# Kernel optimization log

Hardware: AMD Instinct MI355X
Metric: run time of the kernel (lower is better)

The kernel has to match this reference:

```python
import jax, jax.numpy as jnp
import numpy as np

CONTEXT_LENGTH = 4096
INPUT_LENGTH = 1024
N_EMBED = 512
HEAD_SIZE = 64
BATCH = 8


def _prefix_causal_mask(T):
    # A=ones(IL,IL), B=zeros(IL,non), C=ones(non,IL), D=tril(non,non)
    il = INPUT_LENGTH
    non = CONTEXT_LENGTH - il
    top = jnp.concatenate([jnp.ones((il, il)), jnp.zeros((il, non))], axis=1)
    bot = jnp.concatenate([jnp.ones((non, il)), jnp.tril(jnp.ones((non, non)))], axis=1)
    E = jnp.concatenate([top, bot], axis=0)
    return E[:T, :T]


def setup_inputs() -> dict:
    key = jax.random.key(0)
    kx, kq, kk, kv = jax.random.split(key, 4)
    scale = N_EMBED ** -0.5
    return {
        "x": jax.random.normal(kx, (BATCH, CONTEXT_LENGTH, N_EMBED), dtype=jnp.float32),
        "Wq": jax.random.normal(kq, (N_EMBED, HEAD_SIZE), dtype=jnp.float32) * scale,
        "Wk": jax.random.normal(kk, (N_EMBED, HEAD_SIZE), dtype=jnp.float32) * scale,
        "Wv": jax.random.normal(kv, (N_EMBED, HEAD_SIZE), dtype=jnp.float32) * scale,
    }


def reference(x, Wq, Wk, Wv):
    B, T, C = x.shape
    q = x @ Wq  # [B,T,h]
    k = x @ Wk  # [B,T,h]
    v = x @ Wv  # [B,T,h]
    # NOTE: original scales by C**-0.5 with C = n_embed (not head_size)
    wei = jnp.einsum("bth,bsh->bts", q, k) * (C ** -0.5)  # [B,T,T]
    mask = _prefix_causal_mask(T)  # [T,T], 1 = visible
    wei = jnp.where(mask == 0, jnp.float32(-jnp.inf), wei)
    wei = jax.nn.softmax(wei, axis=-1)
    # dropout p=0.0 (eval): identity
    return jnp.einsum("bts,bsh->bth", wei, v)  # [B,T,h]
```

## Files before the change

### kernel.cpp

```cpp
#include <hip/hip_runtime.h>
#include <hip/hip_bf16.h>


typedef short short8 __attribute__((ext_vector_type(8)));
typedef float floatx4 __attribute__((ext_vector_type(4)));

static __device__ __forceinline__ unsigned short f2b(float f) {
  unsigned u = __float_as_uint(f);
  unsigned r = (u + 0x7fffu + ((u >> 16) & 1u)) >> 16;
  return (unsigned short)r;
}

static __device__ __forceinline__ unsigned pkbf(float lo, float hi) {
  __hip_bfloat162 t = __float22bfloat162_rn(make_float2(lo, hi));
  unsigned d;
  __builtin_memcpy(&d, &t, 4);
  return d;
}

union S8U {
  short8 s;
  unsigned u[4];
};

__global__ __launch_bounds__(256) void wtrans(
    const float* __restrict__ Wq, const float* __restrict__ Wk,
    const float* __restrict__ Wv, unsigned short* __restrict__ Wtf) {
  int o = blockIdx.x * 256 + threadIdx.x;
  int e = o & 7;
  int ln = (o >> 3) & 63;
  int jg = o >> 9;
  int ks = jg / 12;
  int j = jg % 12;
  int m = j >> 2;
  int n = (j & 3) * 16 + (ln & 15);
  int k = ks * 32 + (ln >> 4) * 8 + e;
  const float* W = (m == 0) ? Wq : (m == 1) ? Wk : Wv;
  Wtf[o] = f2b(W[k * 64 + n]);
}

__global__ __launch_bounds__(256, 3) void proj(
    const float* __restrict__ x, const unsigned short* __restrict__ Wtf,
    unsigned short* __restrict__ q, unsigned short* __restrict__ Kf,
    unsigned short* __restrict__ Vf) {
  __shared__ float Cc[2][12][16][17];

  const int tid = threadIdx.x;
  const int lane = tid & 63;
  const int w = tid >> 6;
  const int u = lane & 15;
  const int qd = lane >> 4;
  const int pr = w >> 1;
  const int p = w & 1;
  const int g0 = blockIdx.x * 32;

  floatx4 acc[12];
#pragma unroll
  for (int j = 0; j < 12; ++j) acc[j] = (floatx4)0.0f;

  const float* xr = x + (size_t)(g0 + pr * 16 + u) * 512;

  for (int it = 0; it < 8; ++it) {
    const int ks = p + it * 2;
    floatx4 x0 = *reinterpret_cast<const floatx4*>(&xr[ks * 32 + qd * 8]);
    floatx4 x1 = *reinterpret_cast<const floatx4*>(&xr[ks * 32 + qd * 8 + 4]);
    S8U a;
    a.u[0] = pkbf(x0[0], x0[1]);
    a.u[1] = pkbf(x0[2], x0[3]);
    a.u[2] = pkbf(x1[0], x1[1]);
    a.u[3] = pkbf(x1[2], x1[3]);
#pragma unroll
    for (int j = 0; j < 12; ++j) {
      short8 bfr = *reinterpret_cast<const short8*>(&Wtf[(size_t)(ks * 12 + j) * 512 + lane * 8]);
      acc[j] = __builtin_amdgcn_mfma_f32_16x16x32_bf16(a.s, bfr, acc[j], 0, 0, 0);
    }
  }

  if (p == 1) {
#pragma unroll
    for (int j = 0; j < 12; ++j)
#pragma unroll
      for (int r = 0; r < 4; ++r)
        Cc[pr][j][qd * 4 + r][u] = acc[j][r];
  }
  __syncthreads();
  if (p == 0) {
#pragma unroll
    for (int j = 0; j < 12; ++j)
#pragma unroll
      for (int r = 0; r < 4; ++r)
        acc[j][r] += Cc[pr][j][qd * 4 + r][u];

    const float cexp = 0.04419417382415922f * 1.4426950408889634f;
    const int rbase = g0 + pr * 16;
    const int b = rbase >> 12;
    const int t = rbase & 4095;
    const int kt = t >> 6;
    const int sb = ((blockIdx.x & 1) << 1) + pr;
    const int sp = blockIdx.x & 1;
    unsigned short* kfb = Kf + ((size_t)(b * 64 + kt)) * 4096;
    unsigned short* vfb = Vf + ((size_t)(b * 64 + kt)) * 4096;

#pragma unroll
    for (int j = 0; j < 4; ++j)
#pragma unroll
      for (int r = 0; r < 4; ++r) {
        q[(size_t)(rbase + qd * 4 + r) * 64 + j * 16 + u] = f2b(acc[j][r] * cexp);
        {
          int kh = j >> 1;
          int qd_f = ((j & 1) << 1) + (u >> 3);
          kfb[(size_t)(kh * 4 + sb) * 512 + (qd_f * 16 + (qd * 4 + r)) * 8 + (u & 7)] =
              f2b(acc[4 + j][r]);
        }
        {
          int qd_f = pr * 2 + (qd >> 1);
          int e = ((qd & 1) << 2) + r;
          vfb[(size_t)(sp * 4 + j) * 512 + (qd_f * 16 + u) * 8 + e] = f2b(acc[8 + j][r]);
        }
      }
  }
}

__global__ __launch_bounds__(256, 2) void attn(
    const unsigned short* __restrict__ q, const unsigned short* __restrict__ Kf,
    const unsigned short* __restrict__ Vf, float* __restrict__ Op,
    float* __restrict__ Lp) {
  __shared__ unsigned Pb[4][4][64][4];
  __shared__ float OcA[64][68];
  __shared__ float OcB[64][68];
  __shared__ float Lc[4][64];

  const int tid = threadIdx.x;
  const int lane = tid & 63;
  const int w = tid >> 6;
  const int u = lane & 15;
  const int qd = lane >> 4;

  const int bx = blockIdx.x;
  const int b = bx & 7;
  const int s = bx >> 3;

  const int ts = (s * 2200) >> 6;
  const int te = ((s + 1) * 2200) >> 6;

  const unsigned short* qp = q + (size_t)b * 4096 * 64;
  const unsigned short* kfp = Kf + (size_t)b * 64 * 4096;
  const unsigned short* vfp = Vf + (size_t)b * 64 * 4096;

  int qt = 0, cq = 0;
  while (cq + ((qt < 16) ? 16 : (qt + 1)) <= ts) {
    cq += (qt < 16) ? 16 : (qt + 1);
    ++qt;
  }

  int tcur = ts;
  while (tcur < te) {
    const int tq = (qt < 16) ? 16 : (qt + 1);
    const int a = tcur - cq;
    const int bnd = (tq < te - cq) ? tq : (te - cq);
    int k0 = (cq * 64) / 2200;
    while ((((k0 + 1) * 2200) >> 6) <= cq) ++k0;
    const int o = s - k0;
    const int g0 = qt * 64;
    const int diagkt = (qt >= 16) ? qt : -1;

    short8 qB[4][2];
#pragma unroll
    for (int nb = 0; nb < 4; ++nb)
#pragma unroll
      for (int kh = 0; kh < 2; ++kh)
        qB[nb][kh] = *reinterpret_cast<const short8*>(
            &qp[(size_t)(g0 + nb * 16 + u) * 64 + kh * 32 + qd * 8]);

    floatx4 OT[4][4];
#pragma unroll
    for (int mb = 0; mb < 4; ++mb)
#pragma unroll
      for (int nb = 0; nb < 4; ++nb) OT[mb][nb] = (floatx4)0.0f;
    float L[4] = {0.f, 0.f, 0.f, 0.f};

    for (int kt = a + w; kt < bnd; kt += 4) {
      const unsigned short* kb = kfp + (size_t)kt * 4096;
      const unsigned short* vb = vfp + (size_t)kt * 4096;
      short8 kA[8];
#pragma unroll
      for (int f = 0; f < 8; ++f)
        kA[f] = *reinterpret_cast<const short8*>(&kb[(size_t)f * 512 + lane * 8]);
      const bool diag = (kt == diagkt);

#pragma unroll
      for (int sp = 0; sp < 2; ++sp) {
        short8 vA[4];
#pragma unroll
        for (int mb = 0; mb < 4; ++mb)
          vA[mb] = *reinterpret_cast<const short8*>(
              &vb[(size_t)(sp * 4 + mb) * 512 + lane * 8]);

        floatx4 ST[2][4];
#pragma unroll
        for (int sbb = 0; sbb < 2; ++sbb)
#pragma unroll
          for (int nb = 0; nb < 4; ++nb) ST[sbb][nb] = (floatx4)0.0f;
#pragma unroll
        for (int kh = 0; kh < 2; ++kh)
#pragma unroll
          for (int sbb = 0; sbb < 2; ++sbb)
#pragma unroll
            for (int nb = 0; nb < 4; ++nb)
              ST[sbb][nb] = __builtin_amdgcn_mfma_f32_16x16x32_bf16(
                  kA[kh * 4 + sp * 2 + sbb], qB[nb][kh], ST[sbb][nb], 0, 0, 0);

        if (diag) {
#pragma unroll
          for (int sbb = 0; sbb < 2; ++sbb)
#pragma unroll
            for (int nb = 0; nb < 4; ++nb)
#pragma unroll
              for (int r = 0; r < 4; ++r) {
                int sl = (sp * 2 + sbb) * 16 + qd * 4 + r;
                int qr = nb * 16 + u;
                if (sl > qr) ST[sbb][nb][r] = -__builtin_inff();
              }
        }

#pragma unroll
        for (int sbb = 0; sbb < 2; ++sbb)
#pragma unroll
          for (int nb = 0; nb < 4; ++nb) {
#pragma unroll
            for (int r = 0; r < 4; ++r)
              ST[sbb][nb][r] = __builtin_amdgcn_exp2f(ST[sbb][nb][r]);
            L[nb] += (ST[sbb][nb][0] + ST[sbb][nb][1]) + (ST[sbb][nb][2] + ST[sbb][nb][3]);
            unsigned lo = pkbf(ST[sbb][nb][0], ST[sbb][nb][1]);
            unsigned hi = pkbf(ST[sbb][nb][2], ST[sbb][nb][3]);
            int dl = (sbb * 2 + (qd >> 1)) * 16 + u;
            int d0 = (qd & 1) * 2;
            *reinterpret_cast<uint2*>(&Pb[w][nb][dl][d0]) = make_uint2(lo, hi);
          }

#pragma unroll
        for (int nb = 0; nb < 4; ++nb) {
          short8 pB = *reinterpret_cast<const short8*>(&Pb[w][nb][lane][0]);
#pragma unroll
          for (int mb = 0; mb < 4; ++mb)
            OT[mb][nb] = __builtin_amdgcn_mfma_f32_16x16x32_bf16(vA[mb], pB, OT[mb][nb], 0, 0, 0);
        }
      }
    }

#pragma unroll
    for (int nb = 0; nb < 4; ++nb) {
      L[nb] += __shfl_xor(L[nb], 16);
      L[nb] += __shfl_xor(L[nb], 32);
    }
    if (lane < 16) {
#pragma unroll
      for (int nb = 0; nb < 4; ++nb) Lc[w][nb * 16 + lane] = L[nb];
    }

    if (w == 1) {
#pragma unroll
      for (int mb = 0; mb < 4; ++mb)
#pragma unroll
        for (int nb = 0; nb < 4; ++nb)
          *reinterpret_cast<floatx4*>(&OcA[nb * 16 + u][mb * 16 + qd * 4]) = OT[mb][nb];
    }
    if (w == 3) {
#pragma unroll
      for (int mb = 0; mb < 4; ++mb)
#pragma unroll
        for (int nb = 0; nb < 4; ++nb)
          *reinterpret_cast<floatx4*>(&OcB[nb * 16 + u][mb * 16 + qd * 4]) = OT[mb][nb];
    }
    __syncthreads();
    if (w == 0) {
#pragma unroll
      for (int mb = 0; mb < 4; ++mb)
#pragma unroll
        for (int nb = 0; nb < 4; ++nb)
          OT[mb][nb] += *reinterpret_cast<const floatx4*>(&OcA[nb * 16 + u][mb * 16 + qd * 4]);
    }
    if (w == 2) {
#pragma unroll
      for (int mb = 0; mb < 4; ++mb)
#pragma unroll
        for (int nb = 0; nb < 4; ++nb) {
          OT[mb][nb] += *reinterpret_cast<const floatx4*>(&OcB[nb * 16 + u][mb * 16 + qd * 4]);
          *reinterpret_cast<floatx4*>(&OcB[nb * 16 + u][mb * 16 + qd * 4]) = OT[mb][nb];
        }
    }
    __syncthreads();
    if (w == 0) {
#pragma unroll
      for (int mb = 0; mb < 4; ++mb)
#pragma unroll
        for (int nb = 0; nb < 4; ++nb) {
          OT[mb][nb] += *reinterpret_cast<const floatx4*>(&OcB[nb * 16 + u][mb * 16 + qd * 4]);
          *reinterpret_cast<floatx4*>(&OcA[nb * 16 + u][mb * 16 + qd * 4]) = OT[mb][nb];
        }
    }
    __syncthreads();

    {
      int qr = tid >> 2;
      int h0 = (tid & 3) * 16;
      float* op = Op + ((size_t)((b * 64 + qt) * 3 + o)) * 4096 + qr * 64 + h0;
#pragma unroll
      for (int c = 0; c < 4; ++c)
        *reinterpret_cast<floatx4*>(&op[c * 4]) =
            *reinterpret_cast<const floatx4*>(&OcA[qr][h0 + c * 4]);
      if ((tid & 3) == 0) {
        float Ltot = (Lc[0][qr] + Lc[1][qr]) + (Lc[2][qr] + Lc[3][qr]);
        Lp[((size_t)((b * 64 + qt) * 3 + o)) * 64 + qr] = Ltot;
      }
    }
    __syncthreads();

    tcur = cq + bnd;
    if (bnd == tq) { cq += tq; ++qt; }
  }
}

__global__ __launch_bounds__(256) void fold(
    const float* __restrict__ Op, const float* __restrict__ Lp,
    float* __restrict__ out) {
  const int bx = blockIdx.x;
  const int b = bx & 7;
  const int qt = bx >> 3;
  const int cq = (qt < 16) ? 16 * qt : 256 + ((17 + qt) * (qt - 16)) / 2;
  const int tq = (qt < 16) ? 16 : (qt + 1);

  int k0 = (cq * 64) / 2200;
  while ((((k0 + 1) * 2200) >> 6) <= cq) ++k0;
  const int last = cq + tq - 1;
  int k1 = (last * 64) / 2200;
  while ((((k1 + 1) * 2200) >> 6) <= last) ++k1;
  const int n = k1 - k0 + 1;

  const int t = threadIdx.x;
  const int qr = t >> 2;
  const int h0 = (t & 3) * 16;
  const size_t pbase = (size_t)((b * 64 + qt) * 3);

  float Ltot = 0.f;
  for (int o = 0; o < n; ++o) Ltot += Lp[(pbase + o) * 64 + qr];

  floatx4 acc[4];
#pragma unroll
  for (int c = 0; c < 4; ++c) acc[c] = (floatx4)0.0f;
  for (int o = 0; o < n; ++o) {
    const float* src = Op + (pbase + o) * 4096 + qr * 64 + h0;
#pragma unroll
    for (int c = 0; c < 4; ++c)
      acc[c] += *reinterpret_cast<const floatx4*>(&src[c * 4]);
  }

  const float inv = 1.0f / Ltot;
  float* op = out + ((size_t)(b * 4096 + qt * 64 + qr)) * 64 + h0;
#pragma unroll
  for (int c = 0; c < 4; ++c) {
    floatx4 v = acc[c] * inv;
    *reinterpret_cast<floatx4*>(&op[c * 4]) = v;
  }
}

extern "C" void kernel_launch(void* const* d_in, const int* in_sizes, int n_in,
                              void* d_out, int out_size, void* d_ws, size_t ws_size,
                              hipStream_t stream) {
  const float* x  = (const float*)d_in[0];
  const float* Wq = (const float*)d_in[1];
  const float* Wk = (const float*)d_in[2];
  const float* Wv = (const float*)d_in[3];

  unsigned short* ws = (unsigned short*)d_ws;
  unsigned short* Wtf = ws;
  unsigned short* qb = ws + 131072;
  unsigned short* kf = qb + 2097152;
  unsigned short* vf = kf + 2097152;
  float* Op = (float*)(ws + 8388608);
  float* Lp = Op + (size_t)8 * 64 * 3 * 4096;

  wtrans<<<384, 256, 0, stream>>>(Wq, Wk, Wv, Wtf);
  proj<<<1024, 256, 0, stream>>>(x, Wtf, qb, kf, vf);
  attn<<<512, 256, 0, stream>>>(qb, kf, vf, Op, Lp);
  fold<<<512, 256, 0, stream>>>(Op, Lp, (float*)d_out);
}
```

Measured before the change: 153.0 us.

## Fuse split-K fold into attention via last-arriver atomic counter

Removes the separate fold kernel. Query tiles handled by a single work chunk now normalize and write the output directly. For split tiles, each block writes its partial result, and the last block to arrive (tracked by an atomic counter zeroed in wtrans) reduces the partials into the output. This saves a kernel launch and the Op/Lp round trip for unsplit tiles, at the cost of threadfences, an atomic, and a serial reduction tail inside attn.

Result: slower. 335.9 us (+119.5%).

```diff
diff --git a/kernel.cpp b/kernel.cpp
--- a/kernel.cpp
+++ b/kernel.cpp
@@ -25,8 +25,10 @@
 
 __global__ __launch_bounds__(256) void wtrans(
     const float* __restrict__ Wq, const float* __restrict__ Wk,
-    const float* __restrict__ Wv, unsigned short* __restrict__ Wtf) {
+    const float* __restrict__ Wv, unsigned short* __restrict__ Wtf,
+    int* __restrict__ cnt) {
   int o = blockIdx.x * 256 + threadIdx.x;
+  if (o < 512) cnt[o] = 0;
   int e = o & 7;
   int ln = (o >> 3) & 63;
   int jg = o >> 9;
@@ -124,11 +126,12 @@
 __global__ __launch_bounds__(256, 2) void attn(
     const unsigned short* __restrict__ q, const unsigned short* __restrict__ Kf,
     const unsigned short* __restrict__ Vf, float* __restrict__ Op,
-    float* __restrict__ Lp) {
+    float* __restrict__ Lp, int* __restrict__ cnt, float* __restrict__ out) {
   __shared__ unsigned Pb[4][4][64][4];
   __shared__ float OcA[64][68];
   __shared__ float OcB[64][68];
   __shared__ float Lc[4][64];
+  __shared__ int lastf;
 
   const int tid = threadIdx.x;
   const int lane = tid & 63;
@@ -160,6 +163,10 @@
     const int bnd = (tq < te - cq) ? tq : (te - cq);
     int k0 = (cq * 64) / 2200;
     while ((((k0 + 1) * 2200) >> 6) <= cq) ++k0;
+    const int lastt = cq + tq - 1;
+    int k1 = (lastt * 64) / 2200;
+    while ((((k1 + 1) * 2200) >> 6) <= lastt) ++k1;
+    const int n = k1 - k0 + 1;
     const int o = s - k0;
     const int g0 = qt * 64;
     const int diagkt = (qt >= 16) ? qt : -1;
@@ -302,65 +309,60 @@
     __syncthreads();
 
     {
-      int qr = tid >> 2;
-      int h0 = (tid & 3) * 16;
-      float* op = Op + ((size_t)((b * 64 + qt) * 3 + o)) * 4096 + qr * 64 + h0;
-#pragma unroll
-      for (int c = 0; c < 4; ++c)
-        *reinterpret_cast<floatx4*>(&op[c * 4]) =
-            *reinterpret_cast<const floatx4*>(&OcA[qr][h0 + c * 4]);
-      if ((tid & 3) == 0) {
-        float Ltot = (Lc[0][qr] + Lc[1][qr]) + (Lc[2][qr] + Lc[3][qr]);
-        Lp[((size_t)((b * 64 + qt) * 3 + o)) * 64 + qr] = Ltot;
+      const int qr = tid >> 2;
+      const int h0 = (tid & 3) * 16;
+      const float Lown = (Lc[0][qr] + Lc[1][qr]) + (Lc[2][qr] + Lc[3][qr]);
+
+      if (n == 1) {
+        const float inv = 1.0f / Lown;
+        float* op = out + ((size_t)(b * 4096 + g0 + qr)) * 64 + h0;
+#pragma unroll
+        for (int c = 0; c < 4; ++c) {
+          floatx4 v = *reinterpret_cast<const floatx4*>(&OcA[qr][h0 + c * 4]);
+          v *= inv;
+          *reinterpret_cast<floatx4*>(&op[c * 4]) = v;
+        }
+      } else {
+        const size_t pbase = (size_t)((b * 64 + qt) * 3);
+        float* op = Op + (pbase + o) * 4096 + qr * 64 + h0;
+#pragma unroll
+        for (int c = 0; c < 4; ++c)
+          *reinterpret_cast<floatx4*>(&op[c * 4]) =
+              *reinterpret_cast<const floatx4*>(&OcA[qr][h0 + c * 4]);
+        if ((tid & 3) == 0) Lp[(pbase + o) * 64 + qr] = Lown;
+
+        __threadfence();
+        if (tid == 0) lastf = (atomicAdd(&cnt[b * 64 + qt], 1) == n - 1);
+        __syncthreads();
+        if (lastf) {
+          __threadfence();
+          float Ltot = Lown;
+          floatx4 acc[4];
+#pragma unroll
+          for (int c = 0; c < 4; ++c)
+            acc[c] = *reinterpret_cast<const floatx4*>(&OcA[qr][h0 + c * 4]);
+          for (int oo = 0; oo < n; ++oo) {
+            if (oo == o) continue;
+            Ltot += Lp[(pbase + oo) * 64 + qr];
+            const float* src = Op + (pbase + oo) * 4096 + qr * 64 + h0;
+#pragma unroll
+            for (int c = 0; c < 4; ++c)
+              acc[c] += *reinterpret_cast<const floatx4*>(&src[c * 4]);
+          }
+          const float inv = 1.0f / Ltot;
+          float* oq = out + ((size_t)(b * 4096 + g0 + qr)) * 64 + h0;
+#pragma unroll
+          for (int c = 0; c < 4; ++c) {
+            floatx4 v = acc[c] * inv;
+            *reinterpret_cast<floatx4*>(&oq[c * 4]) = v;
+          }
+        }
       }
     }
     __syncthreads();
 
     tcur = cq + bnd;
     if (bnd == tq) { cq += tq; ++qt; }
-  }
-}
-
-__global__ __launch_bounds__(256) void fold(
-    const float* __restrict__ Op, const float* __restrict__ Lp,
-    float* __restrict__ out) {
-  const int bx = blockIdx.x;
-  const int b = bx & 7;
-  const int qt = bx >> 3;
-  const int cq = (qt < 16) ? 16 * qt : 256 + ((17 + qt) * (qt - 16)) / 2;
-  const int tq = (qt < 16) ? 16 : (qt + 1);
-
-  int k0 = (cq * 64) / 2200;
-  while ((((k0 + 1) * 2200) >> 6) <= cq) ++k0;
-  const int last = cq + tq - 1;
-  int k1 = (last * 64) / 2200;
-  while ((((k1 + 1) * 2200) >> 6) <= last) ++k1;
-  const int n = k1 - k0 + 1;
-
-  const int t = threadIdx.x;
-  const int qr = t >> 2;
-  const int h0 = (t & 3) * 16;
-  const size_t pbase = (size_t)((b * 64 + qt) * 3);
-
-  float Ltot = 0.f;
-  for (int o = 0; o < n; ++o) Ltot += Lp[(pbase + o) * 64 + qr];
-
-  floatx4 acc[4];
-#pragma unroll
-  for (int c = 0; c < 4; ++c) acc[c] = (floatx4)0.0f;
-  for (int o = 0; o < n; ++o) {
-    const float* src = Op + (pbase + o) * 4096 + qr * 64 + h0;
-#pragma unroll
-    for (int c = 0; c < 4; ++c)
-      acc[c] += *reinterpret_cast<const floatx4*>(&src[c * 4]);
-  }
-
-  const float inv = 1.0f / Ltot;
-  float* op = out + ((size_t)(b * 4096 + qt * 64 + qr)) * 64 + h0;
-#pragma unroll
-  for (int c = 0; c < 4; ++c) {
-    floatx4 v = acc[c] * inv;
-    *reinterpret_cast<floatx4*>(&op[c * 4]) = v;
   }
 }
 
@@ -379,9 +381,9 @@
   unsigned short* vf = kf + 2097152;
   float* Op = (float*)(ws + 8388608);
   float* Lp = Op + (size_t)8 * 64 * 3 * 4096;
-
-  wtrans<<<384, 256, 0, stream>>>(Wq, Wk, Wv, Wtf);
+  int* cnt = (int*)(Lp + (size_t)8 * 64 * 3 * 64);
+
+  wtrans<<<384, 256, 0, stream>>>(Wq, Wk, Wv, Wtf, cnt);
   proj<<<1024, 256, 0, stream>>>(x, Wtf, qb, kf, vf);
-  attn<<<512, 256, 0, stream>>>(qb, kf, vf, Op, Lp);
-  fold<<<512, 256, 0, stream>>>(Op, Lp, (float*)d_out);
-}
+  attn<<<512, 256, 0, stream>>>(qb, kf, vf, Op, Lp, cnt, (float*)d_out);
+}
```
